# Optimization experiments

Measured on AMD Instinct MI355X. Metric: run time of the kernel, lower is better.

## Reference

```python
import jax, jax.numpy as jnp
import numpy as np

B, L, D, K = 4, 512, 768, 96
H = 4 * D  # projection hidden width


def _proj(x, w1, b1, w2, b2):
    # create_projection_layer: Linear -> ReLU -> (Dropout, identity at eval) -> Linear
    return jnp.maximum(x @ w1 + b1, 0.0) @ w2 + b2


def setup_inputs() -> dict:
    key = jax.random.key(0)
    ks = jax.random.split(key, 12)
    g = lambda k, shape, fan: jax.random.normal(k, shape, jnp.float32) * (1.0 / np.sqrt(fan))
    inp = {
        "h": jax.random.normal(ks[0], (B, L, D), jnp.float32),
        "span_idx": jax.random.randint(ks[1], (B, K, 2), 0, L),
        "ps_w1": g(ks[2], (D, H), D), "ps_b1": jnp.zeros((H,), jnp.float32),
        "ps_w2": g(ks[3], (H, D), H), "ps_b2": jnp.zeros((D,), jnp.float32),
        "pe_w1": g(ks[4], (D, H), D), "pe_b1": jnp.zeros((H,), jnp.float32),
        "pe_w2": g(ks[5], (H, D), H), "pe_b2": jnp.zeros((D,), jnp.float32),
        "so_w1": g(ks[6], (2 * D, H), 2 * D), "so_b1": jnp.zeros((H,), jnp.float32),
        "so_w2": g(ks[7], (H, D), H), "so_b2": jnp.zeros((D,), jnp.float32),
        "ro_w1": g(ks[8], (2 * D, H), 2 * D), "ro_b1": jnp.zeros((H,), jnp.float32),
        "ro_w2": g(ks[9], (H, D), H), "ro_b2": jnp.zeros((D,), jnp.float32),
    }
    return inp


def _gather_tokens(rep, idx):
    # rep: [B,L,D], idx: [B,K] -> [B,K,D]
    b, k = idx.shape
    d = rep.shape[-1]
    return jnp.take_along_axis(rep, jnp.broadcast_to(idx[:, :, None], (b, k, d)), axis=1)


def reference(h, span_idx, ps_w1, ps_b1, ps_w2, ps_b2, pe_w1, pe_b1, pe_w2, pe_b2,
              so_w1, so_b1, so_w2, so_b2, ro_w1, ro_b1, ro_w2, ro_b2):
    # SpanMarkerV1
    start_rep = _proj(h, ps_w1, ps_b1, ps_w2, ps_b2)   # [B,L,D]
    end_rep = _proj(h, pe_w1, pe_b1, pe_w2, pe_b2)     # [B,L,D]
    st = _gather_tokens(start_rep, span_idx[:, :, 0])  # [B,K,D]
    en = _gather_tokens(end_rep, span_idx[:, :, 1])    # [B,K,D]
    cat = jnp.maximum(jnp.concatenate([st, en], axis=-1), 0.0)  # relu
    entity_reps = _proj(cat, so_w1, so_b1, so_w2, so_b2)        # [B,K,D]

    # off-diagonal pair enumeration, row-major (i,j) with i != j — static indices
    n = entity_reps.shape[1]
    idx = np.arange(n)
    ii = np.repeat(idx, n)
    jj = np.tile(idx, n)
    keep = ii != jj
    ii, jj = ii[keep], jj[keep]  # each length n*(n-1)
    pairs = jnp.concatenate([entity_reps[:, ii], entity_reps[:, jj]], axis=-1)  # [B,P,2D]
    return _proj(pairs, ro_w1, ro_b1, ro_w2, ro_b2)  # [B,P,D]
```

## Files before the change

### kernel.cpp

```cpp
#include <hip/hip_runtime.h>
#include <hip/hip_bf16.h>

#define Bdim 4
#define Ldim 512
#define Ddim 768
#define Kspan 96
#define Hdim 3072
#define Pdim 9120
#define MROWS 384
#define NT6 96

typedef __bf16 bf16x8 __attribute__((ext_vector_type(8)));
typedef float f32x4 __attribute__((ext_vector_type(4)));
typedef float f32x16 __attribute__((ext_vector_type(16)));
typedef unsigned short ushort8v __attribute__((ext_vector_type(8)));

static __device__ __forceinline__ unsigned short f2bf(float x){
  return __builtin_bit_cast(unsigned short, (__bf16)x);
}
static __device__ __forceinline__ float bf2f(unsigned short u){
  return (float)__builtin_bit_cast(__bf16, u);
}
static __device__ __forceinline__ float bfbits2f(unsigned short u){
  return __builtin_bit_cast(float, (unsigned)u << 16);
}

struct TJob { const float* W; unsigned short* Th; unsigned short* Tl; int K; int N; int base; };
struct TJobs { TJob j[7]; };

__global__ __launch_bounds__(256) void transpose_multi(TJobs JJ)
{
  int x = blockIdx.x;
  int ji = 0;
  #pragma unroll
  for (int q = 1; q < 7; q++) if (x >= JJ.j[q].base) ji = q;
  TJob J = JJ.j[ji];
  int local = x - J.base;
  int tilesX = J.N >> 6;
  int bx = local % tilesX, by = local / tilesX;
  __shared__ float tile[64][65];
  int k0 = by * 64, n0 = bx * 64;
  int c = threadIdx.x & 63, r0 = threadIdx.x >> 6;
  for (int p = 0; p < 16; p++){
    int r = r0 + p * 4;
    tile[c][r] = J.W[(size_t)(k0 + r) * J.N + n0 + c];
  }
  __syncthreads();
  for (int p = 0; p < 16; p++){
    int n = r0 + p * 4;
    float xv = tile[n][c];
    unsigned short h = f2bf(xv);
    size_t o = (size_t)(n0 + n) * J.K + k0 + c;
    J.Th[o] = h;
    J.Tl[o] = f2bf(xv - bf2f(h));
  }
}

__global__ __launch_bounds__(256) void pack_w2(
    const float* __restrict__ W, unsigned short* __restrict__ W2B)
{
  __shared__ float tile[32][129];
  int kt = blockIdx.x, nq = blockIdx.y, t = threadIdx.x;
  for (int q = 0; q < 16; q++){
    int flat = q * 256 + t;
    int kl = flat >> 7, n = flat & 127;
    tile[kl][n] = W[(size_t)(kt * 32 + kl) * Ddim + nq * 128 + n];
  }
  __syncthreads();
  unsigned short* outp = W2B + (size_t)(nq * 96 + kt) * 4096;
  for (int q = 0; q < 16; q++){
    int o = q * 256 + t;
    int wn = (o >> 11) & 1, kh = (o >> 10) & 1, nf = (o >> 9) & 1;
    int hs = (o >> 8) & 1, l31 = (o >> 3) & 31, e = o & 7;
    int nl = wn * 64 + nf * 32 + l31;
    int kl = (kh * 2 + hs) * 8 + e;
    outp[o] = f2bf(tile[kl][nl]);
  }
}

__global__ __launch_bounds__(256) void gather_rows(
    const float* __restrict__ h, const int* __restrict__ span, float* __restrict__ hg)
{
  int x = blockIdx.x;
  int sel = (x >= MROWS) ? 1 : 0;
  int r = x - sel * MROWS;
  int b = r / Kspan, k = r - b * Kspan;
  int idx = span[(b * Kspan + k) * 2 + sel];
  const float* src = h + ((size_t)b * Ldim + idx) * Ddim;
  float* dst = hg + (size_t)x * Ddim;
  for (int d = threadIdx.x; d < Ddim; d += 256) dst[d] = src[d];
}

struct GJob {
  const float* A;
  const unsigned short* Wh;
  const unsigned short* Wl;
  const float* bias;
  float* C;
};

template<int MODE, int SPLIT>
__global__ __launch_bounds__(256) void gemm_ms(
    GJob j0, GJob j1, int ldA, int ldW, int ldC, int kLen, size_t csz)
{
  constexpr int SR = 40;
  __shared__ __align__(16) unsigned short Ah[64 * SR], Al[64 * SR];
  __shared__ __align__(16) unsigned short Bh[128 * SR], Bl[128 * SR];
  int zj, s;
  if (SPLIT == 1){ zj = blockIdx.z; s = 0; }
  else { zj = blockIdx.z / SPLIT; s = blockIdx.z % SPLIT; }
  const GJob J = zj ? j1 : j0;
  int kBegin = s * kLen;
  float* Cptr = (MODE == 2) ? (J.C + (size_t)s * csz) : J.C;

  int m0 = blockIdx.y * 64, n0 = blockIdx.x * 128;
  int t = threadIdx.x, lane = t & 63, wid = t >> 6;
  int wm = wid >> 1, wn = wid & 1;
  int lr = lane & 15, lk = (lane >> 4) * 8;
  f32x4 acc[2][4] = {};
  int ar = t >> 2, akq = t & 3;
  for (int k0 = 0; k0 < kLen; k0 += 32){
    {
      const float* sp = J.A + (size_t)(m0 + ar) * ldA + kBegin + k0 + akq * 8;
      f32x4 x0 = *(const f32x4*)sp, x1 = *(const f32x4*)(sp + 4);
      ushort8v vh, vl;
      for (int e = 0; e < 4; e++){ float x = x0[e]; unsigned short hh = f2bf(x); vh[e] = hh; vl[e] = f2bf(x - bf2f(hh)); }
      for (int e = 0; e < 4; e++){ float x = x1[e]; unsigned short hh = f2bf(x); vh[e+4] = hh; vl[e+4] = f2bf(x - bf2f(hh)); }
      *(ushort8v*)&Ah[ar * SR + akq * 8] = vh;
      *(ushort8v*)&Al[ar * SR + akq * 8] = vl;
    }
    for (int p = 0; p < 2; p++){
      int idx = p * 256 + t; int n = idx >> 2, kq = idx & 3;
      size_t go = (size_t)(n0 + n) * ldW + kBegin + k0 + kq * 8;
      *(ushort8v*)&Bh[n * SR + kq * 8] = *(const ushort8v*)(J.Wh + go);
      *(ushort8v*)&Bl[n * SR + kq * 8] = *(const ushort8v*)(J.Wl + go);
    }
    __syncthreads();
    bf16x8 ah[2], al2[2], bh[4], bl[4];
    for (int f = 0; f < 2; f++){ int o = (wm * 32 + f * 16 + lr) * SR + lk; ah[f] = *(const bf16x8*)&Ah[o]; al2[f] = *(const bf16x8*)&Al[o]; }
    for (int g = 0; g < 4; g++){ int o = (wn * 64 + g * 16 + lr) * SR + lk; bh[g] = *(const bf16x8*)&Bh[o]; bl[g] = *(const bf16x8*)&Bl[o]; }
    for (int f = 0; f < 2; f++)
      for (int g = 0; g < 4; g++){
        acc[f][g] = __builtin_amdgcn_mfma_f32_16x16x32_bf16(ah[f],  bh[g], acc[f][g], 0, 0, 0);
        acc[f][g] = __builtin_amdgcn_mfma_f32_16x16x32_bf16(ah[f],  bl[g], acc[f][g], 0, 0, 0);
        acc[f][g] = __builtin_amdgcn_mfma_f32_16x16x32_bf16(al2[f], bh[g], acc[f][g], 0, 0, 0);
      }
    __syncthreads();
  }
  int rr = (lane >> 4) * 4;
  for (int f = 0; f < 2; f++){
    int gm = m0 + wm * 32 + f * 16 + rr;
    for (int g = 0; g < 4; g++){
      int gn = n0 + wn * 64 + g * 16 + (lane & 15);
      float bv = (MODE != 2 && J.bias) ? J.bias[gn] : 0.f;
      for (int r2 = 0; r2 < 4; r2++){
        float v = acc[f][g][r2] + bv;
        if (MODE == 0) v = fmaxf(v, 0.f);
        if (MODE == 6){
          ((unsigned short*)J.C)[(size_t)(gm + r2) * ldC + gn] = f2bf(v);
        } else {
          Cptr[(size_t)(gm + r2) * ldC + gn] = v;
        }
      }
    }
  }
}

template<bool RELU>
__global__ __launch_bounds__(256) void reduce_part(
    const float* __restrict__ P, int S,
    const float* __restrict__ bias0, const float* __restrict__ bias1,
    float* __restrict__ outp, int zCount, int ldOut)
{
  const int MN = MROWS * Ddim;
  int idx4 = blockIdx.x * 256 + threadIdx.x;
  int flat = idx4 * 4;
  if (flat >= MN * zCount) return;
  int z = flat / MN; int rem = flat - z * MN;
  int r = rem / Ddim; int c = rem - r * Ddim;
  const float* base = P + (size_t)z * S * MN + rem;
  f32x4 sv = *(const f32x4*)base;
  for (int ss = 1; ss < S; ss++){ f32x4 v = *(const f32x4*)(base + (size_t)ss * MN); sv += v; }
  const float* bp = z ? bias1 : bias0;
  f32x4 bv = *(const f32x4*)(bp + c);
  sv += bv;
  if (RELU) for (int e = 0; e < 4; e++) sv[e] = fmaxf(sv[e], 0.f);
  *(f32x4*)(outp + (size_t)r * ldOut + z * Ddim + c) = sv;
}

__global__ __launch_bounds__(256, 2) void pair_gemm9(
    const unsigned short* __restrict__ Ub,
    const unsigned short* __restrict__ Vp,
    const unsigned short* __restrict__ W2B,
    const float* __restrict__ b2,
    float* __restrict__ out)
{
  __shared__ __align__(16) unsigned short As[2][192 * 32];

  int x = blockIdx.x;
  int xcd = x & 7;
  int s = x >> 3;
  int grp = s / 48;
  int ig  = s - grp * 48;
  int combo = xcd + grp * 8;
  int nq = combo % 6, b = combo / 6;

  int t = threadIdx.x, lane = t & 63, w = t >> 6;
  int wm = w >> 1, wn = w & 1;
  int l31 = lane & 31, hsel = lane >> 5;
  int i0 = ig * 2, i = i0 + wm;

  int brow = t >> 2, bg = t & 3;
  bool hiMid = (brow >= 32);
  int vj0 = brow;
  int vj1 = hiMid ? (brow - 32) : (brow + 64);
  int vj2 = brow + 32;

  f32x16 acc[3][2] = {};
  ushort8v vA0, vA1, vA2, uA0, uA1;
  ushort8v vB0, vB1, vB2, uB0, uB1;

  const unsigned short* Vbase = Vp + (size_t)(b * 96) * Hdim + bg * 8;
  const unsigned short* Ubase = Ub + (size_t)(b * 96 + i0) * Hdim + bg * 8;
  const unsigned short* Wt = W2B + (size_t)(nq * 96) * 4096 + wn * 2048 + hsel * 256 + l31 * 8;
  unsigned short* const As0 = &As[0][0];
  unsigned short* const As1 = &As[1][0];

  #define LOADVU(KT, V0, V1, V2, U0, U1) { \
    int koff = (KT) * 32; \
    V0 = *(const ushort8v*)(Vbase + (size_t)vj0 * Hdim + koff); \
    V1 = *(const ushort8v*)(Vbase + (size_t)vj1 * Hdim + koff); \
    V2 = *(const ushort8v*)(Vbase + (size_t)vj2 * Hdim + koff); \
    U0 = *(const ushort8v*)(Ubase + koff); \
    U1 = *(const ushort8v*)(Ubase + Hdim + koff); \
  }
  #define LOADB(KT, BB) { \
    const unsigned short* p_ = Wt + (size_t)(KT) * 4096; \
    BB[0] = *(const ushort8v*)(p_); \
    BB[1] = *(const ushort8v*)(p_ + 512); \
    BB[2] = *(const ushort8v*)(p_ + 1024); \
    BB[3] = *(const ushort8v*)(p_ + 1536); \
  }
  #define BUILD(DP, V0, V1, V2, U0, U1) { \
    ushort8v um_ = hiMid ? (U1) : (U0); \
    _Pragma("unroll") \
    for (int q = 0; q < 3; q++){ \
      int r_ = brow + 64 * q; \
      ushort8v uu = (q == 0) ? (U0) : ((q == 2) ? (U1) : um_); \
      ushort8v vv = (q == 0) ? (V0) : ((q == 2) ? (V2) : (V1)); \
      ushort8v pk; \
      _Pragma("unroll") \
      for (int e = 0; e < 8; e++) \
        pk[e] = f2bf(fmaxf(bfbits2f(uu[e]) + bfbits2f(vv[e]), 0.f)); \
      *(ushort8v*)((DP) + r_ * 32 + ((bg ^ ((r_ >> 1) & 3)) << 3)) = pk; \
    } \
  }

  auto compute = [&](const unsigned short* ap, const ushort8v* bfrag){
    #pragma unroll
    for (int kh = 0; kh < 2; kh++){
      int g = kh * 2 + hsel;
      bf16x8 afr[3];
      #pragma unroll
      for (int mf = 0; mf < 3; mf++){
        int r = wm * 96 + mf * 32 + l31;
        afr[mf] = *(const bf16x8*)(ap + r * 32 + ((g ^ ((r >> 1) & 3)) << 3));
      }
      #pragma unroll
      for (int mf = 0; mf < 3; mf++)
        #pragma unroll
        for (int nf = 0; nf < 2; nf++)
          acc[mf][nf] = __builtin_amdgcn_mfma_f32_32x32x16_bf16(
              afr[mf], __builtin_bit_cast(bf16x8, bfrag[kh * 2 + nf]), acc[mf][nf], 0, 0, 0);
    }
  };

  LOADVU(0, vA0, vA1, vA2, uA0, uA1);
  LOADVU(1, vB0, vB1, vB2, uB0, uB1);
  BUILD(As0, vA0, vA1, vA2, uA0, uA1);
  __syncthreads();

  for (int kt = 0; kt < NT6; kt += 2){
    {
      ushort8v bb[4];
      LOADB(kt, bb);
      if (kt + 2 < NT6) LOADVU(kt + 2, vA0, vA1, vA2, uA0, uA1);
      if (kt + 1 < NT6) BUILD(As1, vB0, vB1, vB2, uB0, uB1);
      compute(As0, bb);
      __syncthreads();
    }
    {
      int ko = kt + 1;
      ushort8v bb[4];
      LOADB(ko, bb);
      if (ko + 2 < NT6) LOADVU(ko + 2, vB0, vB1, vB2, uB0, uB1);
      if (ko + 1 < NT6) BUILD(As0, vA0, vA1, vA2, uA0, uA1);
      compute(As1, bb);
      __syncthreads();
    }
  }

  size_t outB = (size_t)b * Pdim;
  int colbase = nq * 128 + wn * 64;
  float bc[2];
  #pragma unroll
  for (int nf = 0; nf < 2; nf++) bc[nf] = b2[colbase + nf * 32 + l31];
  #pragma unroll
  for (int mf = 0; mf < 3; mf++){
    #pragma unroll
    for (int reg = 0; reg < 16; reg++){
      int j = mf * 32 + (reg & 3) + 8 * (reg >> 2) + 4 * hsel;
      if (j == i) continue;
      int p = i * 95 + j - (j > i ? 1 : 0);
      float* orow = out + (outB + p) * Ddim + colbase;
      #pragma unroll
      for (int nf = 0; nf < 2; nf++)
        orow[nf * 32 + l31] = acc[mf][nf][reg] + bc[nf];
    }
  }
  #undef LOADVU
  #undef LOADB
  #undef BUILD
}

extern "C" void kernel_launch(void* const* d_in, const int* in_sizes, int n_in,
                              void* d_out, int out_size, void* d_ws, size_t ws_size,
                              hipStream_t stream)
{
  (void)in_sizes; (void)n_in; (void)out_size;
  const float* h     = (const float*)d_in[0];
  const int*   span  = (const int*)d_in[1];
  const float* ps_w1 = (const float*)d_in[2];
  const float* ps_b1 = (const float*)d_in[3];
  const float* ps_w2 = (const float*)d_in[4];
  const float* ps_b2 = (const float*)d_in[5];
  const float* pe_w1 = (const float*)d_in[6];
  const float* pe_b1 = (const float*)d_in[7];
  const float* pe_w2 = (const float*)d_in[8];
  const float* pe_b2 = (const float*)d_in[9];
  const float* so_w1 = (const float*)d_in[10];
  const float* so_b1 = (const float*)d_in[11];
  const float* so_w2 = (const float*)d_in[12];
  const float* so_b2 = (const float*)d_in[13];
  const float* ro_w1 = (const float*)d_in[14];
  const float* ro_b1 = (const float*)d_in[15];
  const float* ro_w2 = (const float*)d_in[16];
  const float* ro_b2 = (const float*)d_in[17];

  char* ws = (char*)d_ws;
  size_t off = 0;
  auto alloc_us = [&](size_t n)->unsigned short*{
    unsigned short* p = (unsigned short*)(ws + off);
    off += ((n * 2 + 255) & ~(size_t)255);
    return p;
  };
  auto alloc_f = [&](size_t n)->float*{
    float* p = (float*)(ws + off);
    off += ((n * 4 + 255) & ~(size_t)255);
    return p;
  };

  unsigned short* ps1h = alloc_us((size_t)Hdim * Ddim); unsigned short* ps1l = alloc_us((size_t)Hdim * Ddim);
  unsigned short* ps2h = alloc_us((size_t)Ddim * Hdim); unsigned short* ps2l = alloc_us((size_t)Ddim * Hdim);
  unsigned short* pe1h = alloc_us((size_t)Hdim * Ddim); unsigned short* pe1l = alloc_us((size_t)Hdim * Ddim);
  unsigned short* pe2h = alloc_us((size_t)Ddim * Hdim); unsigned short* pe2l = alloc_us((size_t)Ddim * Hdim);
  unsigned short* so1h = alloc_us((size_t)Hdim * 2 * Ddim); unsigned short* so1l = alloc_us((size_t)Hdim * 2 * Ddim);
  unsigned short* so2h = alloc_us((size_t)Ddim * Hdim); unsigned short* so2l = alloc_us((size_t)Ddim * Hdim);
  unsigned short* ro1h = alloc_us((size_t)Hdim * 2 * Ddim); unsigned short* ro1l = alloc_us((size_t)Hdim * 2 * Ddim);
  unsigned short* W2B  = alloc_us((size_t)6 * 96 * 4096);
  unsigned short* Vp   = alloc_us((size_t)MROWS * Hdim);
  unsigned short* Ub   = alloc_us((size_t)MROWS * Hdim);
  float* hg     = alloc_f((size_t)2 * MROWS * Ddim);
  float* mid_s  = alloc_f((size_t)MROWS * Hdim);
  float* mid_e  = alloc_f((size_t)MROWS * Hdim);
  float* cat    = alloc_f((size_t)MROWS * 2 * Ddim);
  float* entity = alloc_f((size_t)MROWS * Ddim);
  const size_t MN = (size_t)MROWS * Ddim;
  float* P2 = alloc_f(8 * MN);
  float* P3 = alloc_f(8 * MN);
  if (off > ws_size) return;

  dim3 tb(256);

  {
    TJobs JJ;
    int base = 0;
    auto add = [&](int idx, const float* W, unsigned short* Th, unsigned short* Tl, int K, int N){
      JJ.j[idx] = TJob{W, Th, Tl, K, N, base};
      base += (N / 64) * (K / 64);
    };
    add(0, ps_w1, ps1h, ps1l, Ddim, Hdim);
    add(1, ps_w2, ps2h, ps2l, Hdim, Ddim);
    add(2, pe_w1, pe1h, pe1l, Ddim, Hdim);
    add(3, pe_w2, pe2h, pe2l, Hdim, Ddim);
    add(4, so_w1, so1h, so1l, 2 * Ddim, Hdim);
    add(5, so_w2, so2h, so2l, Hdim, Ddim);
    add(6, ro_w1, ro1h, ro1l, 2 * Ddim, Hdim);
    transpose_multi<<<base, tb, 0, stream>>>(JJ);
  }
  pack_w2<<<dim3(NT6, 6), tb, 0, stream>>>(ro_w2, W2B);

  gather_rows<<<2 * MROWS, tb, 0, stream>>>(h, span, hg);

  {
    GJob j0{hg,                      ps1h, ps1l, ps_b1, mid_s};
    GJob j1{hg + (size_t)MROWS*Ddim, pe1h, pe1l, pe_b1, mid_e};
    gemm_ms<0,1><<<dim3(Hdim/128, MROWS/64, 2), tb, 0, stream>>>(j0, j1, Ddim, Ddim, Hdim, Ddim, 0);
  }
  {
    GJob j0{mid_s, ps2h, ps2l, nullptr, P2};
    GJob j1{mid_e, pe2h, pe2l, nullptr, P2 + 4*MN};
    gemm_ms<2,4><<<dim3(Ddim/128, MROWS/64, 8), tb, 0, stream>>>(j0, j1, Hdim, Hdim, Ddim, Hdim/4, MN);
  }
  reduce_part<true><<<(2*(int)MN)/1024, tb, 0, stream>>>(P2, 4, ps_b2, pe_b2, cat, 2, 2*Ddim);
  {
    GJob j0{cat, so1h, so1l, so_b1, mid_s};
    gemm_ms<0,1><<<dim3(Hdim/128, MROWS/64, 1), tb, 0, stream>>>(j0, j0, 2*Ddim, 2*Ddim, Hdim, 2*Ddim, 0);
  }
  {
    GJob j0{mid_s, so2h, so2l, nullptr, P3};
    gemm_ms<2,8><<<dim3(Ddim/128, MROWS/64, 8), tb, 0, stream>>>(j0, j0, Hdim, Hdim, Ddim, Hdim/8, MN);
  }
  reduce_part<false><<<((int)MN)/1024, tb, 0, stream>>>(P3, 8, so_b2, so_b2, entity, 1, Ddim);
  {
    GJob j0{entity, ro1h,        ro1l,        ro_b1,  (float*)Ub};
    GJob j1{entity, ro1h + Ddim, ro1l + Ddim, nullptr, (float*)Vp};
    gemm_ms<6,1><<<dim3(Hdim/128, MROWS/64, 2), tb, 0, stream>>>(j0, j1, Ddim, 2*Ddim, Hdim, Ddim, 0);
  }

  pair_gemm9<<<1152, tb, 0, stream>>>(Ub, Vp, W2B, ro_b2, (float*)d_out);
}
```

Measured before the change: 463.0 us.

## Pre-pack V into MFMA fragment layout and build A fragments in registers

Adds a pack_v_frag kernel that rearranges the bf16 V matrix into MFMA-fragment order, so the pair GEMM can load A-side V fragments directly per lane. The pair GEMM drops its shared-memory A tile, double-buffered LDS build and __syncthreads, and instead forms relu(U_i + V_j) fragments in registers before each MFMA. The intent is to remove LDS traffic and barriers from the main loop. In exchange it adds one small kernel launch, and each wave now reads V itself instead of sharing a tile across the block, which raises global/L2 reads and register pressure.

```diff
diff --git a/kernel.cpp b/kernel.cpp
--- a/kernel.cpp
+++ b/kernel.cpp
@@ -75,6 +75,23 @@
     int nl = wn * 64 + nf * 32 + l31;
     int kl = (kh * 2 + hs) * 8 + e;
     outp[o] = f2bf(tile[kl][nl]);
+  }
+}
+
+__global__ __launch_bounds__(256) void pack_v_frag(
+    const unsigned short* __restrict__ Vb, unsigned short* __restrict__ Vpk)
+{
+  int kt = blockIdx.x, b = blockIdx.y, t = threadIdx.x;
+  unsigned short* outp = Vpk + (size_t)(b * 96 + kt) * 3072;
+  #pragma unroll
+  for (int q = 0; q < 12; q++){
+    int o = q * 256 + t;
+    int kh = o / 1536;
+    int rem = o - kh * 1536;
+    int mf = rem >> 9;
+    int rem2 = rem & 511;
+    int hsel = rem2 >> 8, l31 = (rem2 >> 3) & 31, e = rem2 & 7;
+    outp[o] = Vb[(size_t)(b * 96 + mf * 32 + l31) * Hdim + kt * 32 + (kh * 2 + hsel) * 8 + e];
   }
 }
 
@@ -188,15 +205,13 @@
   *(f32x4*)(outp + (size_t)r * ldOut + z * Ddim + c) = sv;
 }
 
-__global__ __launch_bounds__(256, 2) void pair_gemm9(
+__global__ __launch_bounds__(256, 2) void pair_gemm10(
     const unsigned short* __restrict__ Ub,
-    const unsigned short* __restrict__ Vp,
+    const unsigned short* __restrict__ Vpk,
     const unsigned short* __restrict__ W2B,
     const float* __restrict__ b2,
     float* __restrict__ out)
 {
-  __shared__ __align__(16) unsigned short As[2][192 * 32];
-
   int x = blockIdx.x;
   int xcd = x & 7;
   int s = x >> 3;
@@ -208,97 +223,102 @@
   int t = threadIdx.x, lane = t & 63, w = t >> 6;
   int wm = w >> 1, wn = w & 1;
   int l31 = lane & 31, hsel = lane >> 5;
-  int i0 = ig * 2, i = i0 + wm;
-
-  int brow = t >> 2, bg = t & 3;
-  bool hiMid = (brow >= 32);
-  int vj0 = brow;
-  int vj1 = hiMid ? (brow - 32) : (brow + 64);
-  int vj2 = brow + 32;
+  int i = ig * 2 + wm;
 
   f32x16 acc[3][2] = {};
-  ushort8v vA0, vA1, vA2, uA0, uA1;
-  ushort8v vB0, vB1, vB2, uB0, uB1;
-
-  const unsigned short* Vbase = Vp + (size_t)(b * 96) * Hdim + bg * 8;
-  const unsigned short* Ubase = Ub + (size_t)(b * 96 + i0) * Hdim + bg * 8;
-  const unsigned short* Wt = W2B + (size_t)(nq * 96) * 4096 + wn * 2048 + hsel * 256 + l31 * 8;
-  unsigned short* const As0 = &As[0][0];
-  unsigned short* const As1 = &As[1][0];
-
-  #define LOADVU(KT, V0, V1, V2, U0, U1) { \
-    int koff = (KT) * 32; \
-    V0 = *(const ushort8v*)(Vbase + (size_t)vj0 * Hdim + koff); \
-    V1 = *(const ushort8v*)(Vbase + (size_t)vj1 * Hdim + koff); \
-    V2 = *(const ushort8v*)(Vbase + (size_t)vj2 * Hdim + koff); \
-    U0 = *(const ushort8v*)(Ubase + koff); \
-    U1 = *(const ushort8v*)(Ubase + Hdim + koff); \
-  }
-  #define LOADB(KT, BB) { \
-    const unsigned short* p_ = Wt + (size_t)(KT) * 4096; \
-    BB[0] = *(const ushort8v*)(p_); \
-    BB[1] = *(const ushort8v*)(p_ + 512); \
-    BB[2] = *(const ushort8v*)(p_ + 1024); \
-    BB[3] = *(const ushort8v*)(p_ + 1536); \
-  }
-  #define BUILD(DP, V0, V1, V2, U0, U1) { \
-    ushort8v um_ = hiMid ? (U1) : (U0); \
-    _Pragma("unroll") \
-    for (int q = 0; q < 3; q++){ \
-      int r_ = brow + 64 * q; \
-      ushort8v uu = (q == 0) ? (U0) : ((q == 2) ? (U1) : um_); \
-      ushort8v vv = (q == 0) ? (V0) : ((q == 2) ? (V2) : (V1)); \
-      ushort8v pk; \
-      _Pragma("unroll") \
-      for (int e = 0; e < 8; e++) \
-        pk[e] = f2bf(fmaxf(bfbits2f(uu[e]) + bfbits2f(vv[e]), 0.f)); \
-      *(ushort8v*)((DP) + r_ * 32 + ((bg ^ ((r_ >> 1) & 3)) << 3)) = pk; \
-    } \
-  }
-
-  auto compute = [&](const unsigned short* ap, const ushort8v* bfrag){
+
+  const unsigned short* Vt = Vpk + (size_t)(b * 96) * 3072 + lane * 8;
+  const unsigned short* Wt = W2B + (size_t)(nq * 96) * 4096 + wn * 2048 + lane * 8;
+  const unsigned short* Ut = Ub + (size_t)(b * 96 + i) * Hdim + hsel * 8;
+
+  ushort8v vE0, vE1, vE2, vE3, vE4, vE5, uE0, uE1;
+  ushort8v vO0, vO1, vO2, vO3, vO4, vO5, uO0, uO1;
+
+  #define LOADV_(KT, V0, V1, V2, V3, V4, V5) { \
+    const unsigned short* p_ = Vt + (size_t)(KT) * 3072; \
+    V0 = *(const ushort8v*)(p_);        V1 = *(const ushort8v*)(p_ + 512); \
+    V2 = *(const ushort8v*)(p_ + 1024); V3 = *(const ushort8v*)(p_ + 1536); \
+    V4 = *(const ushort8v*)(p_ + 2048); V5 = *(const ushort8v*)(p_ + 2560); \
+  }
+  #define LOADU_(KT, U0, U1) { \
+    const unsigned short* p_ = Ut + (KT) * 32; \
+    U0 = *(const ushort8v*)(p_); U1 = *(const ushort8v*)(p_ + 16); \
+  }
+
+  auto mkfrag = [&](ushort8v v, ushort8v u) -> bf16x8 {
+    ushort8v pk;
     #pragma unroll
-    for (int kh = 0; kh < 2; kh++){
-      int g = kh * 2 + hsel;
-      bf16x8 afr[3];
-      #pragma unroll
-      for (int mf = 0; mf < 3; mf++){
-        int r = wm * 96 + mf * 32 + l31;
-        afr[mf] = *(const bf16x8*)(ap + r * 32 + ((g ^ ((r >> 1) & 3)) << 3));
-      }
-      #pragma unroll
-      for (int mf = 0; mf < 3; mf++)
-        #pragma unroll
-        for (int nf = 0; nf < 2; nf++)
-          acc[mf][nf] = __builtin_amdgcn_mfma_f32_32x32x16_bf16(
-              afr[mf], __builtin_bit_cast(bf16x8, bfrag[kh * 2 + nf]), acc[mf][nf], 0, 0, 0);
-    }
+    for (int e = 0; e < 8; e++)
+      pk[e] = f2bf(fmaxf(bfbits2f(v[e]) + bfbits2f(u[e]), 0.f));
+    return __builtin_bit_cast(bf16x8, pk);
   };
 
-  LOADVU(0, vA0, vA1, vA2, uA0, uA1);
-  LOADVU(1, vB0, vB1, vB2, uB0, uB1);
-  BUILD(As0, vA0, vA1, vA2, uA0, uA1);
-  __syncthreads();
+  LOADV_(0, vE0, vE1, vE2, vE3, vE4, vE5);
+  LOADU_(0, uE0, uE1);
 
   for (int kt = 0; kt < NT6; kt += 2){
     {
-      ushort8v bb[4];
-      LOADB(kt, bb);
-      if (kt + 2 < NT6) LOADVU(kt + 2, vA0, vA1, vA2, uA0, uA1);
-      if (kt + 1 < NT6) BUILD(As1, vB0, vB1, vB2, uB0, uB1);
-      compute(As0, bb);
-      __syncthreads();
+      const unsigned short* wp = Wt + (size_t)kt * 4096;
+      ushort8v b0 = *(const ushort8v*)(wp);
+      ushort8v b1 = *(const ushort8v*)(wp + 512);
+      ushort8v b2v = *(const ushort8v*)(wp + 1024);
+      ushort8v b3 = *(const ushort8v*)(wp + 1536);
+      LOADV_(kt + 1, vO0, vO1, vO2, vO3, vO4, vO5);
+      LOADU_(kt + 1, uO0, uO1);
+      bf16x8 a;
+      a = mkfrag(vE0, uE0);
+      acc[0][0] = __builtin_amdgcn_mfma_f32_32x32x16_bf16(a, __builtin_bit_cast(bf16x8, b0), acc[0][0], 0, 0, 0);
+      acc[0][1] = __builtin_amdgcn_mfma_f32_32x32x16_bf16(a, __builtin_bit_cast(bf16x8, b1), acc[0][1], 0, 0, 0);
+      a = mkfrag(vE1, uE0);
+      acc[1][0] = __builtin_amdgcn_mfma_f32_32x32x16_bf16(a, __builtin_bit_cast(bf16x8, b0), acc[1][0], 0, 0, 0);
+      acc[1][1] = __builtin_amdgcn_mfma_f32_32x32x16_bf16(a, __builtin_bit_cast(bf16x8, b1), acc[1][1], 0, 0, 0);
+      a = mkfrag(vE2, uE0);
+      acc[2][0] = __builtin_amdgcn_mfma_f32_32x32x16_bf16(a, __builtin_bit_cast(bf16x8, b0), acc[2][0], 0, 0, 0);
+      acc[2][1] = __builtin_amdgcn_mfma_f32_32x32x16_bf16(a, __builtin_bit_cast(bf16x8, b1), acc[2][1], 0, 0, 0);
+      a = mkfrag(vE3, uE1);
+      acc[0][0] = __builtin_amdgcn_mfma_f32_32x32x16_bf16(a, __builtin_bit_cast(bf16x8, b2v), acc[0][0], 0, 0, 0);
+      acc[0][1] = __builtin_amdgcn_mfma_f32_32x32x16_bf16(a, __builtin_bit_cast(bf16x8, b3), acc[0][1], 0, 0, 0);
+      a = mkfrag(vE4, uE1);
+      acc[1][0] = __builtin_amdgcn_mfma_f32_32x32x16_bf16(a, __builtin_bit_cast(bf16x8, b2v), acc[1][0], 0, 0, 0);
+      acc[1][1] = __builtin_amdgcn_mfma_f32_32x32x16_bf16(a, __builtin_bit_cast(bf16x8, b3), acc[1][1], 0, 0, 0);
+      a = mkfrag(vE5, uE1);
+      acc[2][0] = __builtin_amdgcn_mfma_f32_32x32x16_bf16(a, __builtin_bit_cast(bf16x8, b2v), acc[2][0], 0, 0, 0);
+      acc[2][1] = __builtin_amdgcn_mfma_f32_32x32x16_bf16(a, __builtin_bit_cast(bf16x8, b3), acc[2][1], 0, 0, 0);
     }
     {
       int ko = kt + 1;
-      ushort8v bb[4];
-      LOADB(ko, bb);
-      if (ko + 2 < NT6) LOADVU(ko + 2, vB0, vB1, vB2, uB0, uB1);
-      if (ko + 1 < NT6) BUILD(As0, vA0, vA1, vA2, uA0, uA1);
-      compute(As1, bb);
-      __syncthreads();
-    }
-  }
+      const unsigned short* wp = Wt + (size_t)ko * 4096;
+      ushort8v b0 = *(const ushort8v*)(wp);
+      ushort8v b1 = *(const ushort8v*)(wp + 512);
+      ushort8v b2v = *(const ushort8v*)(wp + 1024);
+      ushort8v b3 = *(const ushort8v*)(wp + 1536);
+      if (ko + 1 < NT6){
+        LOADV_(ko + 1, vE0, vE1, vE2, vE3, vE4, vE5);
+        LOADU_(ko + 1, uE0, uE1);
+      }
+      bf16x8 a;
+      a = mkfrag(vO0, uO0);
+      acc[0][0] = __builtin_amdgcn_mfma_f32_32x32x16_bf16(a, __builtin_bit_cast(bf16x8, b0), acc[0][0], 0, 0, 0);
+      acc[0][1] = __builtin_amdgcn_mfma_f32_32x32x16_bf16(a, __builtin_bit_cast(bf16x8, b1), acc[0][1], 0, 0, 0);
+      a = mkfrag(vO1, uO0);
+      acc[1][0] = __builtin_amdgcn_mfma_f32_32x32x16_bf16(a, __builtin_bit_cast(bf16x8, b0), acc[1][0], 0, 0, 0);
+      acc[1][1] = __builtin_amdgcn_mfma_f32_32x32x16_bf16(a, __builtin_bit_cast(bf16x8, b1), acc[1][1], 0, 0, 0);
+      a = mkfrag(vO2, uO0);
+      acc[2][0] = __builtin_amdgcn_mfma_f32_32x32x16_bf16(a, __builtin_bit_cast(bf16x8, b0), acc[2][0], 0, 0, 0);
+      acc[2][1] = __builtin_amdgcn_mfma_f32_32x32x16_bf16(a, __builtin_bit_cast(bf16x8, b1), acc[2][1], 0, 0, 0);
+      a = mkfrag(vO3, uO1);
+      acc[0][0] = __builtin_amdgcn_mfma_f32_32x32x16_bf16(a, __builtin_bit_cast(bf16x8, b2v), acc[0][0], 0, 0, 0);
+      acc[0][1] = __builtin_amdgcn_mfma_f32_32x32x16_bf16(a, __builtin_bit_cast(bf16x8, b3), acc[0][1], 0, 0, 0);
+      a = mkfrag(vO4, uO1);
+      acc[1][0] = __builtin_amdgcn_mfma_f32_32x32x16_bf16(a, __builtin_bit_cast(bf16x8, b2v), acc[1][0], 0, 0, 0);
+      acc[1][1] = __builtin_amdgcn_mfma_f32_32x32x16_bf16(a, __builtin_bit_cast(bf16x8, b3), acc[1][1], 0, 0, 0);
+      a = mkfrag(vO5, uO1);
+      acc[2][0] = __builtin_amdgcn_mfma_f32_32x32x16_bf16(a, __builtin_bit_cast(bf16x8, b2v), acc[2][0], 0, 0, 0);
+      acc[2][1] = __builtin_amdgcn_mfma_f32_32x32x16_bf16(a, __builtin_bit_cast(bf16x8, b3), acc[2][1], 0, 0, 0);
+    }
+  }
+  #undef LOADV_
+  #undef LOADU_
 
   size_t outB = (size_t)b * Pdim;
   int colbase = nq * 128 + wn * 64;
@@ -318,9 +338,6 @@
         orow[nf * 32 + l31] = acc[mf][nf][reg] + bc[nf];
     }
   }
-  #undef LOADVU
-  #undef LOADB
-  #undef BUILD
 }
 
 extern "C" void kernel_launch(void* const* d_in, const int* in_sizes, int n_in,
@@ -369,7 +386,8 @@
   unsigned short* ro1h = alloc_us((size_t)Hdim * 2 * Ddim); unsigned short* ro1l = alloc_us((size_t)Hdim * 2 * Ddim);
   unsigned short* W2B  = alloc_us((size_t)6 * 96 * 4096);
   unsigned short* Vp   = alloc_us((size_t)MROWS * Hdim);
-  unsigned short* Ub   = alloc_us((size_t)MROWS * Hdim);
+  unsigned short* Ubf  = alloc_us((size_t)MROWS * Hdim);
+  unsigned short* Vpk  = alloc_us((size_t)MROWS * Hdim);
   float* hg     = alloc_f((size_t)2 * MROWS * Ddim);
   float* mid_s  = alloc_f((size_t)MROWS * Hdim);
   float* mid_e  = alloc_f((size_t)MROWS * Hdim);
@@ -423,10 +441,11 @@
   }
   reduce_part<false><<<((int)MN)/1024, tb, 0, stream>>>(P3, 8, so_b2, so_b2, entity, 1, Ddim);
   {
-    GJob j0{entity, ro1h,        ro1l,        ro_b1,  (float*)Ub};
+    GJob j0{entity, ro1h,        ro1l,        ro_b1,  (float*)Ubf};
     GJob j1{entity, ro1h + Ddim, ro1l + Ddim, nullptr, (float*)Vp};
     gemm_ms<6,1><<<dim3(Hdim/128, MROWS/64, 2), tb, 0, stream>>>(j0, j1, Ddim, 2*Ddim, Hdim, Ddim, 0);
   }
-
-  pair_gemm9<<<1152, tb, 0, stream>>>(Ub, Vp, W2B, ro_b2, (float*)d_out);
-}
+  pack_v_frag<<<dim3(NT6, Bdim), tb, 0, stream>>>(Vp, Vpk);
+
+  pair_gemm10<<<1152, tb, 0, stream>>>(Ubf, Vpk, W2B, ro_b2, (float*)d_out);
+}
```

Result: slower. 472.7 us (+2.1%).
